# Kernel optimization log

Measured on AMD Instinct MI355X. Metric: run time of the kernel, lower is better.

The kernel has to match this reference:

```python
import jax, jax.numpy as jnp
import numpy as np

IN_CHANNELS = 64
OUT_CHANNELS = 64
SEQ_LEN = 512
KERNEL_SIZE = 9
STRIDE = 1
PADDING = 4  # symmetric
OUT_SEQ_LEN = (SEQ_LEN + 2 * PADDING - (KERNEL_SIZE - 1) - 1) // STRIDE + 1  # 512


def setup_inputs() -> dict:
    key = jax.random.key(0)
    k1, k2, k3 = jax.random.split(key, 3)
    x = jax.random.normal(k1, (64, IN_CHANNELS, SEQ_LEN), dtype=jnp.float32)
    # nn.init.normal_(std=0.1)
    weight = 0.1 * jax.random.normal(k2, (IN_CHANNELS, OUT_CHANNELS, KERNEL_SIZE, OUT_SEQ_LEN), dtype=jnp.float32)
    bias = 0.1 * jax.random.normal(k3, (OUT_CHANNELS, OUT_SEQ_LEN), dtype=jnp.float32)
    return {"x": x, "weight": weight, "bias": bias}


def reference(x, weight, bias):
    # x: [B, Ci, S] -> pad last dim
    xp = jnp.pad(x, ((0, 0), (0, 0), (PADDING, PADDING)))
    # Unfold (im2col) as a gather: same math as the one-hot grouped conv.
    starts = jnp.arange(OUT_SEQ_LEN) * STRIDE            # [L]
    offs = jnp.arange(KERNEL_SIZE)                        # [K]
    idx = starts[:, None] + offs[None, :]                 # [L, K]
    patches = xp[:, :, idx]                               # [B, Ci, L, K]
    # per-position matmul: 'b i l k, i o k l -> b o l'
    out = jnp.einsum('bilk,iokl->bol', patches, weight)
    out = out + bias                                      # [B, Co, L]
    return out
```

## Files before the change

kernel.cpp:

```cpp
#include <hip/hip_runtime.h>


#define CIN   64
#define COUT  64
#define SEQ   512
#define KS    9
#define LT    32
#define OT    16
#define BT    16
#define LWIN  40
#define XSTR  72
#define XLW   (BT*XSTR)
#define BOSTR 42
#define BLSTR (OT*BOSTR + 2)
#define NCHUNK 18
#define WSTRIDE (COUT*KS*SEQ)
#define XS_ELEMS (LWIN*XLW)
#define BS_ELEMS (LT*BLSTR)
#define LDS_BYTES ((XS_ELEMS + BS_ELEMS)*2)

typedef __attribute__((ext_vector_type(8))) short bf16x8;
typedef __attribute__((ext_vector_type(4))) float f32x4;

__device__ __forceinline__ ushort f2bf(float f) {
    return (ushort)((__float_as_uint(f) + 0x8000u) >> 16);
}
__device__ __forceinline__ uint pack2bf(float a0, float a1) {
    uint u0 = __float_as_uint(a0) + 0x8000u;
    uint u1 = __float_as_uint(a1) + 0x8000u;
    return __builtin_amdgcn_perm(u1, u0, 0x07060302);
}

__global__ __launch_bounds__(256, 1)
void lc1d_mfma(const float* __restrict__ x, const float* __restrict__ w,
               const float* __restrict__ bias, float* __restrict__ out)
{
    extern __shared__ ushort lds[];
    ushort* Xs = lds;
    ushort* Bs = lds + XS_ELEMS;

    const int tid  = threadIdx.x;
    const int lane = tid & 63;
    const int wv   = tid >> 6;
    const int lt  = blockIdx.x >> 2;
    const int os  = blockIdx.x & 3;
    const int bsp = blockIdx.y;
    const int l0 = lt * LT;
    const int o0 = os * OT;
    const int b0 = bsp * BT;

    const int lq = tid & 7;
    const int oo = (tid >> 3) & 15;
    const int pp = tid >> 7;

    const float* wbase = w + ((size_t)(o0 + oo) * KS) * SEQ + l0 + lq * 4;

    float4 pfA[16], pfB[16];

    #define LOAD_CHUNK(pf, c) {                                                  \
        const int kq_ = (c) >> 1, ih_ = (c) & 1;                                 \
        const float* p_ = wbase + (size_t)kq_ * SEQ                              \
                          + (size_t)(ih_*32 + pp*16) * WSTRIDE;                  \
        _Pragma("unroll")                                                        \
        for (int p8 = 0; p8 < 8; ++p8) {                                         \
            pf[2*p8]   = *(const float4*)(p_ + (size_t)(2*p8  ) * WSTRIDE);      \
            pf[2*p8+1] = *(const float4*)(p_ + (size_t)(2*p8+1) * WSTRIDE);      \
        }                                                                        \
    }

    #define WRITE_BS(pf) {                                                       \
        _Pragma("unroll")                                                        \
        for (int p8 = 0; p8 < 8; ++p8) {                                         \
            const int m_ = pp*8 + p8;                                            \
            ushort* dst_ = Bs + oo*BOSTR + 2*m_ + lq*4*BLSTR;                    \
            _Pragma("unroll")                                                    \
            for (int dl = 0; dl < 4; ++dl) {                                     \
                uint pk_ = pack2bf((&pf[2*p8].x)[dl], (&pf[2*p8+1].x)[dl]);      \
                *(uint*)(dst_ + dl*BLSTR) = pk_;                                 \
            }                                                                    \
        }                                                                        \
    }

    LOAD_CHUNK(pfA, 0)
    LOAD_CHUNK(pfB, 1)

    #pragma unroll
    for (int it = 0; it < 40; ++it) {
        int flat = tid + 256*it;
        int row = flat / 10;
        int q   = flat - row*10;
        int b = row >> 6, i = row & 63;
        const float* src = x + ((size_t)((b0 + b)*CIN + i))*SEQ + (l0 - 4) + q*4;
        float4 v = make_float4(0.f, 0.f, 0.f, 0.f);
        if (!((lt == 0 && q == 0) || (lt == 15 && q == 9)))
            v = *(const float4*)src;
        ushort* dst = Xs + (q*4)*XLW + b*XSTR + i;
        dst[0*XLW] = f2bf(v.x);
        dst[1*XLW] = f2bf(v.y);
        dst[2*XLW] = f2bf(v.z);
        dst[3*XLW] = f2bf(v.w);
    }

    f32x4 acc[8];
    #pragma unroll
    for (int j = 0; j < 8; ++j) acc[j] = (f32x4)0.0f;

    const int aoff = (lane & 15)*XSTR + (lane >> 4)*8;
    const int boff = (lane & 15)*BOSTR + (lane >> 4)*8;

    __syncthreads();

    #define DO_MFMA(c) {                                                         \
        const int kq_ = (c) >> 1, ih_ = (c) & 1;                                 \
        const ushort* Ab_ = Xs + (wv*8 + kq_)*XLW + ih_*32 + aoff;               \
        const ushort* Bb_ = Bs + (wv*8)*BLSTR + boff;                            \
        _Pragma("unroll")                                                        \
        for (int j = 0; j < 8; ++j) {                                            \
            bf16x8 Af_ = *(const bf16x8*)(Ab_ + j*XLW);                          \
            const uint* bw_ = (const uint*)(Bb_ + j*BLSTR);                      \
            uint4 bu_ = make_uint4(bw_[0], bw_[1], bw_[2], bw_[3]);              \
            bf16x8 Bf_ = __builtin_bit_cast(bf16x8, bu_);                        \
            acc[j] = __builtin_amdgcn_mfma_f32_16x16x32_bf16(Af_, Bf_, acc[j],   \
                                                             0, 0, 0);           \
        }                                                                        \
    }

    for (int cc = 0; cc < NCHUNK; cc += 2) {
        WRITE_BS(pfA)
        __syncthreads();
        if (cc + 2 < NCHUNK) LOAD_CHUNK(pfA, cc + 2)
        DO_MFMA(cc)
        __syncthreads();

        WRITE_BS(pfB)
        __syncthreads();
        if (cc + 3 < NCHUNK) LOAD_CHUNK(pfB, cc + 3)
        DO_MFMA(cc + 1)
        __syncthreads();
    }

    const int orow = o0 + (lane & 15);
    const int rgrp = lane >> 4;
    #pragma unroll
    for (int j = 0; j < 8; ++j) {
        int l = l0 + wv*8 + j;
        float bv = bias[orow*SEQ + l];
        #pragma unroll
        for (int r = 0; r < 4; ++r) {
            int b = b0 + rgrp*4 + r;
            out[(size_t)(b*COUT + orow)*SEQ + l] = acc[j][r] + bv;
        }
    }
}

extern "C" void kernel_launch(void* const* d_in, const int* in_sizes, int n_in,
                              void* d_out, int out_size, void* d_ws, size_t ws_size,
                              hipStream_t stream) {
    const float* x    = (const float*)d_in[0];
    const float* wgt  = (const float*)d_in[1];
    const float* bias = (const float*)d_in[2];
    float* out        = (float*)d_out;

    hipFuncSetAttribute((const void*)lc1d_mfma,
                        hipFuncAttributeMaxDynamicSharedMemorySize, LDS_BYTES);
    dim3 grid(64, 4);
    lc1d_mfma<<<grid, 256, LDS_BYTES, stream>>>(x, wgt, bias, out);
}
```

Baseline: 163.1 us.

## Halve sequence tile and double threads per block for more parallelism

Shrinks the sequence tile from 32 to 16 positions and raises the block from 256 to 512 threads, doubling the grid to 512 blocks. Each thread now prefetches 4 float4 weight vectors per chunk instead of 16, and each wave computes 2 MFMA accumulators instead of 8. The aim is to spread the weight-bandwidth-bound streaming over more CUs and waves and to cut register pressure. In exchange, each block's x halo is a larger fraction of its input window, and there are more barriers relative to compute.

```diff
diff --git a/kernel.cpp b/kernel.cpp
--- a/kernel.cpp
+++ b/kernel.cpp
@@ -5,10 +5,10 @@
 #define COUT  64
 #define SEQ   512
 #define KS    9
-#define LT    32
+#define LT    16
 #define OT    16
 #define BT    16
-#define LWIN  40
+#define LWIN  24
 #define XSTR  72
 #define XLW   (BT*XSTR)
 #define BOSTR 42
@@ -31,7 +31,7 @@
     return __builtin_amdgcn_perm(u1, u0, 0x07060302);
 }
 
-__global__ __launch_bounds__(256, 1)
+__global__ __launch_bounds__(512, 4)
 void lc1d_mfma(const float* __restrict__ x, const float* __restrict__ w,
                const float* __restrict__ bias, float* __restrict__ out)
 {
@@ -49,34 +49,30 @@
     const int o0 = os * OT;
     const int b0 = bsp * BT;
 
-    const int lq = tid & 7;
-    const int oo = (tid >> 3) & 15;
-    const int pp = tid >> 7;
+    const int lq = tid & 3;
+    const int oo = (tid >> 2) & 15;
+    const int ig = tid >> 6;
 
     const float* wbase = w + ((size_t)(o0 + oo) * KS) * SEQ + l0 + lq * 4;
 
-    float4 pfA[16], pfB[16];
+    float4 pfA[4], pfB[4];
 
     #define LOAD_CHUNK(pf, c) {                                                  \
         const int kq_ = (c) >> 1, ih_ = (c) & 1;                                 \
         const float* p_ = wbase + (size_t)kq_ * SEQ                              \
-                          + (size_t)(ih_*32 + pp*16) * WSTRIDE;                  \
+                          + (size_t)(ih_*32 + ig*4) * WSTRIDE;                   \
         _Pragma("unroll")                                                        \
-        for (int p8 = 0; p8 < 8; ++p8) {                                         \
-            pf[2*p8]   = *(const float4*)(p_ + (size_t)(2*p8  ) * WSTRIDE);      \
-            pf[2*p8+1] = *(const float4*)(p_ + (size_t)(2*p8+1) * WSTRIDE);      \
-        }                                                                        \
+        for (int q = 0; q < 4; ++q)                                              \
+            pf[q] = *(const float4*)(p_ + (size_t)q * WSTRIDE);                  \
     }
 
     #define WRITE_BS(pf) {                                                       \
         _Pragma("unroll")                                                        \
-        for (int p8 = 0; p8 < 8; ++p8) {                                         \
-            const int m_ = pp*8 + p8;                                            \
-            ushort* dst_ = Bs + oo*BOSTR + 2*m_ + lq*4*BLSTR;                    \
+        for (int s = 0; s < 2; ++s) {                                            \
             _Pragma("unroll")                                                    \
             for (int dl = 0; dl < 4; ++dl) {                                     \
-                uint pk_ = pack2bf((&pf[2*p8].x)[dl], (&pf[2*p8+1].x)[dl]);      \
-                *(uint*)(dst_ + dl*BLSTR) = pk_;                                 \
+                uint pk_ = pack2bf((&pf[2*s].x)[dl], (&pf[2*s+1].x)[dl]);        \
+                *(uint*)(Bs + (lq*4+dl)*BLSTR + oo*BOSTR + ig*4 + 2*s) = pk_;    \
             }                                                                    \
         }                                                                        \
     }
@@ -85,14 +81,14 @@
     LOAD_CHUNK(pfB, 1)
 
     #pragma unroll
-    for (int it = 0; it < 40; ++it) {
-        int flat = tid + 256*it;
-        int row = flat / 10;
-        int q   = flat - row*10;
+    for (int it = 0; it < 12; ++it) {
+        int flat = tid + 512*it;
+        int row = flat / 6;
+        int q   = flat - row*6;
         int b = row >> 6, i = row & 63;
         const float* src = x + ((size_t)((b0 + b)*CIN + i))*SEQ + (l0 - 4) + q*4;
         float4 v = make_float4(0.f, 0.f, 0.f, 0.f);
-        if (!((lt == 0 && q == 0) || (lt == 15 && q == 9)))
+        if (!((lt == 0 && q == 0) || (lt == 31 && q == 5)))
             v = *(const float4*)src;
         ushort* dst = Xs + (q*4)*XLW + b*XSTR + i;
         dst[0*XLW] = f2bf(v.x);
@@ -101,27 +97,26 @@
         dst[3*XLW] = f2bf(v.w);
     }
 
-    f32x4 acc[8];
-    #pragma unroll
-    for (int j = 0; j < 8; ++j) acc[j] = (f32x4)0.0f;
+    f32x4 acc[2];
+    acc[0] = (f32x4)0.0f;
+    acc[1] = (f32x4)0.0f;
 
-    const int aoff = (lane & 15)*XSTR + (lane >> 4)*8;
+    const int aoff = (lane & 15)*XSTR  + (lane >> 4)*8;
     const int boff = (lane & 15)*BOSTR + (lane >> 4)*8;
 
     __syncthreads();
 
     #define DO_MFMA(c) {                                                         \
         const int kq_ = (c) >> 1, ih_ = (c) & 1;                                 \
-        const ushort* Ab_ = Xs + (wv*8 + kq_)*XLW + ih_*32 + aoff;               \
-        const ushort* Bb_ = Bs + (wv*8)*BLSTR + boff;                            \
         _Pragma("unroll")                                                        \
-        for (int j = 0; j < 8; ++j) {                                            \
-            bf16x8 Af_ = *(const bf16x8*)(Ab_ + j*XLW);                          \
-            const uint* bw_ = (const uint*)(Bb_ + j*BLSTR);                      \
+        for (int jr = 0; jr < 2; ++jr) {                                         \
+            const int r_ = wv*2 + jr;                                            \
+            bf16x8 Af_ = *(const bf16x8*)(Xs + (r_ + kq_)*XLW + ih_*32 + aoff);  \
+            const uint* bw_ = (const uint*)(Bs + r_*BLSTR + boff);               \
             uint4 bu_ = make_uint4(bw_[0], bw_[1], bw_[2], bw_[3]);              \
             bf16x8 Bf_ = __builtin_bit_cast(bf16x8, bu_);                        \
-            acc[j] = __builtin_amdgcn_mfma_f32_16x16x32_bf16(Af_, Bf_, acc[j],   \
-                                                             0, 0, 0);           \
+            acc[jr] = __builtin_amdgcn_mfma_f32_16x16x32_bf16(Af_, Bf_, acc[jr], \
+                                                              0, 0, 0);          \
         }                                                                        \
     }
 
@@ -142,13 +137,13 @@
     const int orow = o0 + (lane & 15);
     const int rgrp = lane >> 4;
     #pragma unroll
-    for (int j = 0; j < 8; ++j) {
-        int l = l0 + wv*8 + j;
+    for (int jr = 0; jr < 2; ++jr) {
+        int l = l0 + wv*2 + jr;
         float bv = bias[orow*SEQ + l];
         #pragma unroll
         for (int r = 0; r < 4; ++r) {
             int b = b0 + rgrp*4 + r;
-            out[(size_t)(b*COUT + orow)*SEQ + l] = acc[j][r] + bv;
+            out[(size_t)(b*COUT + orow)*SEQ + l] = acc[jr][r] + bv;
         }
     }
 }
@@ -163,6 +158,6 @@
 
     hipFuncSetAttribute((const void*)lc1d_mfma,
                         hipFuncAttributeMaxDynamicSharedMemorySize, LDS_BYTES);
-    dim3 grid(64, 4);
-    lc1d_mfma<<<grid, 256, LDS_BYTES, stream>>>(x, wgt, bias, out);
+    dim3 grid(128, 4);
+    lc1d_mfma<<<grid, 512, LDS_BYTES, stream>>>(x, wgt, bias, out);
 }
```

New measurement: 162.9 us. Within noise of the previous version (-0.1%).
